# Kernel optimization log

Measured on AMD Instinct MI355X. Metric: run time of the kernel, lower is better.

Reference implementation:

```python
import jax, jax.numpy as jnp
import numpy as np

B, N, DIN, DOUT = 8192, 4, 1024, 256

def setup_inputs() -> dict:
    key = jax.random.key(0)
    k1, k2, k3, k4 = jax.random.split(key, 4)
    adj = jax.random.uniform(k1, (N, N), dtype=jnp.float32)
    features = jax.random.normal(k2, (B, N, DIN), dtype=jnp.float32)
    # nn.Linear(input_size, output_size): weight [DOUT, DIN], bias [DOUT]
    bound = 1.0 / np.sqrt(DIN)
    W = jax.random.uniform(k3, (DOUT, DIN), dtype=jnp.float32, minval=-bound, maxval=bound)
    b = jax.random.uniform(k4, (DOUT,), dtype=jnp.float32, minval=-bound, maxval=bound)
    return {"adj": adj, "features": features, "W": W, "b": b}

def reference(adj, features, W, b):
    # Batched equivalent of: for i in B: linear(adj @ features[i]) -> [B, 4, DOUT]
    h = jnp.einsum("nm,bmf->bnf", adj, features)  # [B, N, DIN]
    return jnp.einsum("bnf,of->bno", h, W) + b    # [B, N, DOUT]
```

## Files before the change

### kernel.cpp

```cpp
#include <hip/hip_runtime.h>


#define DIN 1024
#define DOUT 256
#define BM 32
#define KI 16
#define LDB 72
#define A_HALFS (BM * LDB)

typedef __bf16 bf16x8 __attribute__((ext_vector_type(8)));
typedef float f32x4 __attribute__((ext_vector_type(4)));
typedef unsigned short u16x8 __attribute__((ext_vector_type(8)));

__device__ __forceinline__ unsigned short f2bf(float f) {
  union { float f; unsigned int u; } v;
  v.f = f;
  unsigned int u = v.u;
  u += 0x7fffu + ((u >> 16) & 1u);
  return (unsigned short)(u >> 16);
}

__global__ __launch_bounds__(256) void wprep_kernel(
    const float* __restrict__ W, unsigned short* __restrict__ ws) {
  const int t = blockIdx.x * 256 + threadIdx.x;
  const int lane = t & 63;
  const int j = (t >> 6) & 3;
  const int ks = (t >> 8) & 1;
  const int kb = (t >> 9) & 15;
  const int g = (t >> 13) & 3;
  const int col = g * 64 + j * 16 + (lane & 15);
  const int k0 = kb * 64 + ks * 32 + (lane >> 4) * 8;
  const f32x4* src = (const f32x4*)(W + (size_t)col * DIN + k0);
  f32x4 a = src[0], b = src[1];
  u16x8 pk;
#pragma unroll
  for (int m = 0; m < 4; ++m) {
    pk[m] = f2bf(a[m]);
    pk[4 + m] = f2bf(b[m]);
  }
  *(u16x8*)(ws + (size_t)t * 8) = pk;
}

__global__ __launch_bounds__(256, 4) void gconv_kernel(
    const float* __restrict__ adj, const float* __restrict__ feat,
    const unsigned short* __restrict__ wbf, const float* __restrict__ bias,
    float* __restrict__ out) {
  __shared__ __align__(16) unsigned short sA[2][A_HALFS];

  const int tid = threadIdx.x;
  const int bM = blockIdx.x * BM;

  const int row0 = tid >> 3;
  const int kc8 = (tid & 7) * 8;
  const float* aptr = feat + (size_t)(bM + row0) * DIN + kc8;
  unsigned short* sw0 = &sA[0][row0 * LDB + kc8];
  unsigned short* sw1 = &sA[1][row0 * LDB + kc8];

  const int lane = tid & 63;
  const int wid = tid >> 6;
  const int wc = wid * 64;
  const int rl = lane & 15;
  const int q = lane >> 4;
  const int q8 = q * 8;

  const unsigned short* bp = wbf + (size_t)wid * 128 * 512 + lane * 8;

  f32x4 acc[2][4];
#pragma unroll
  for (int i = 0; i < 2; ++i)
#pragma unroll
    for (int j = 0; j < 4; ++j) acc[i][j] = f32x4{0.f, 0.f, 0.f, 0.f};

  f32x4 pa0 = *(const f32x4*)aptr;
  f32x4 pa1 = *(const f32x4*)(aptr + 4);
  {
    u16x8 pk;
#pragma unroll
    for (int m = 0; m < 4; ++m) {
      pk[m] = f2bf(pa0[m]);
      pk[4 + m] = f2bf(pa1[m]);
    }
    *(u16x8*)sw0 = pk;
  }
  pa0 = *(const f32x4*)(aptr + 64);
  pa1 = *(const f32x4*)(aptr + 68);

  for (int kb = 0; kb < KI; ++kb) {
    bf16x8 bfr[2][4];
#pragma unroll
    for (int ks = 0; ks < 2; ++ks)
#pragma unroll
      for (int j = 0; j < 4; ++j)
        bfr[ks][j] = *(const bf16x8*)(bp + ((kb * 2 + ks) * 4 + j) * 512);

    __builtin_amdgcn_sched_barrier(0);
    asm volatile("s_waitcnt lgkmcnt(0)" ::: "memory");
    __builtin_amdgcn_s_barrier();
    __builtin_amdgcn_sched_barrier(0);

    const unsigned short* sa = (kb & 1) ? &sA[1][0] : &sA[0][0];
#pragma unroll
    for (int ks = 0; ks < 2; ++ks) {
      const int ko = ks * 32 + q8;
      bf16x8 af[2];
#pragma unroll
      for (int i = 0; i < 2; ++i)
        af[i] = *(const bf16x8*)(sa + (i * 16 + rl) * LDB + ko);
#pragma unroll
      for (int i = 0; i < 2; ++i)
#pragma unroll
        for (int j = 0; j < 4; ++j)
          acc[i][j] = __builtin_amdgcn_mfma_f32_16x16x32_bf16(
              af[i], bfr[ks][j], acc[i][j], 0, 0, 0);
    }

    if (kb + 1 < KI) {
      u16x8 pk;
#pragma unroll
      for (int m = 0; m < 4; ++m) {
        pk[m] = f2bf(pa0[m]);
        pk[4 + m] = f2bf(pa1[m]);
      }
      unsigned short* sw = ((kb + 1) & 1) ? sw1 : sw0;
      *(u16x8*)sw = pk;
      if (kb + 2 < KI) {
        const float* a0 = aptr + (size_t)(kb + 2) * 64;
        pa0 = *(const f32x4*)a0;
        pa1 = *(const f32x4*)(a0 + 4);
      }
    }
  }

  float am[16];
#pragma unroll
  for (int i = 0; i < 16; ++i) am[i] = adj[i];

  float bv[4];
#pragma unroll
  for (int j = 0; j < 4; ++j) bv[j] = bias[wc + j * 16 + rl];

#pragma unroll
  for (int i = 0; i < 2; ++i) {
    const size_t rowbase = (size_t)(bM + i * 16 + q * 4);
#pragma unroll
    for (int j = 0; j < 4; ++j) {
      const int col = wc + j * 16 + rl;
      float* op = out + rowbase * DOUT + col;
      f32x4 g = acc[i][j];
#pragma unroll
      for (int n = 0; n < 4; ++n) {
        op[(size_t)n * DOUT] = am[n * 4 + 0] * g[0] + am[n * 4 + 1] * g[1] +
                               am[n * 4 + 2] * g[2] + am[n * 4 + 3] * g[3] +
                               bv[j];
      }
    }
  }
}

extern "C" void kernel_launch(void* const* d_in, const int* in_sizes, int n_in,
                              void* d_out, int out_size, void* d_ws,
                              size_t ws_size, hipStream_t stream) {
  const float* adj = (const float*)d_in[0];
  const float* feat = (const float*)d_in[1];
  const float* W = (const float*)d_in[2];
  const float* bias = (const float*)d_in[3];
  float* out = (float*)d_out;
  unsigned short* ws = (unsigned short*)d_ws;

  wprep_kernel<<<128, 256, 0, stream>>>(W, ws);
  gconv_kernel<<<8192 * 4 / BM, 256, 0, stream>>>(adj, feat, ws, bias, out);
}
```

Baseline: 223.3 us.

## Give each wave a private A tile to remove block-wide barriers

Each wave now loads, converts to bf16, and stores the full 32-row feature tile into its own double-buffered LDS region, so the per-iteration block-wide s_barrier is removed. The intent is to let waves run their MMA loops without synchronizing with each other. In exchange, every block reads and converts the same feature data four times, LDS usage grows fourfold, and launch bounds drop to three blocks per CU.

```diff
diff --git a/kernel.cpp b/kernel.cpp
--- a/kernel.cpp
+++ b/kernel.cpp
@@ -20,6 +20,16 @@
   return (unsigned short)(u >> 16);
 }
 
+__device__ __forceinline__ u16x8 pack8(f32x4 lo, f32x4 hi) {
+  u16x8 r;
+#pragma unroll
+  for (int m = 0; m < 4; ++m) {
+    r[m] = f2bf(lo[m]);
+    r[4 + m] = f2bf(hi[m]);
+  }
+  return r;
+}
+
 __global__ __launch_bounds__(256) void wprep_kernel(
     const float* __restrict__ W, unsigned short* __restrict__ ws) {
   const int t = blockIdx.x * 256 + threadIdx.x;
@@ -32,29 +42,17 @@
   const int k0 = kb * 64 + ks * 32 + (lane >> 4) * 8;
   const f32x4* src = (const f32x4*)(W + (size_t)col * DIN + k0);
   f32x4 a = src[0], b = src[1];
-  u16x8 pk;
-#pragma unroll
-  for (int m = 0; m < 4; ++m) {
-    pk[m] = f2bf(a[m]);
-    pk[4 + m] = f2bf(b[m]);
-  }
-  *(u16x8*)(ws + (size_t)t * 8) = pk;
+  *(u16x8*)(ws + (size_t)t * 8) = pack8(a, b);
 }
 
-__global__ __launch_bounds__(256, 4) void gconv_kernel(
+__global__ __launch_bounds__(256, 3) void gconv_kernel(
     const float* __restrict__ adj, const float* __restrict__ feat,
     const unsigned short* __restrict__ wbf, const float* __restrict__ bias,
     float* __restrict__ out) {
-  __shared__ __align__(16) unsigned short sA[2][A_HALFS];
+  __shared__ __align__(16) unsigned short sA[4][2][A_HALFS];
 
   const int tid = threadIdx.x;
   const int bM = blockIdx.x * BM;
-
-  const int row0 = tid >> 3;
-  const int kc8 = (tid & 7) * 8;
-  const float* aptr = feat + (size_t)(bM + row0) * DIN + kc8;
-  unsigned short* sw0 = &sA[0][row0 * LDB + kc8];
-  unsigned short* sw1 = &sA[1][row0 * LDB + kc8];
 
   const int lane = tid & 63;
   const int wid = tid >> 6;
@@ -62,6 +60,11 @@
   const int rl = lane & 15;
   const int q = lane >> 4;
   const int q8 = q * 8;
+
+  const int arow = lane >> 3;
+  const int ac8 = (lane & 7) * 8;
+  const float* abase = feat + (size_t)(bM + arow) * DIN + ac8;
+  unsigned short* swl = &sA[wid][0][arow * LDB + ac8];
 
   const unsigned short* bp = wbf + (size_t)wid * 128 * 512 + lane * 8;
 
@@ -71,19 +74,20 @@
 #pragma unroll
     for (int j = 0; j < 4; ++j) acc[i][j] = f32x4{0.f, 0.f, 0.f, 0.f};
 
-  f32x4 pa0 = *(const f32x4*)aptr;
-  f32x4 pa1 = *(const f32x4*)(aptr + 4);
-  {
-    u16x8 pk;
+  f32x4 pf[4][2];
 #pragma unroll
-    for (int m = 0; m < 4; ++m) {
-      pk[m] = f2bf(pa0[m]);
-      pk[4 + m] = f2bf(pa1[m]);
-    }
-    *(u16x8*)sw0 = pk;
+  for (int v = 0; v < 4; ++v) {
+    pf[v][0] = *(const f32x4*)(abase + (size_t)v * 8 * DIN);
+    pf[v][1] = *(const f32x4*)(abase + (size_t)v * 8 * DIN + 4);
   }
-  pa0 = *(const f32x4*)(aptr + 64);
-  pa1 = *(const f32x4*)(aptr + 68);
+#pragma unroll
+  for (int v = 0; v < 4; ++v)
+    *(u16x8*)(swl + v * 8 * LDB) = pack8(pf[v][0], pf[v][1]);
+#pragma unroll
+  for (int v = 0; v < 4; ++v) {
+    pf[v][0] = *(const f32x4*)(abase + (size_t)v * 8 * DIN + 64);
+    pf[v][1] = *(const f32x4*)(abase + (size_t)v * 8 * DIN + 68);
+  }
 
   for (int kb = 0; kb < KI; ++kb) {
     bf16x8 bfr[2][4];
@@ -93,40 +97,36 @@
       for (int j = 0; j < 4; ++j)
         bfr[ks][j] = *(const bf16x8*)(bp + ((kb * 2 + ks) * 4 + j) * 512);
 
-    __builtin_amdgcn_sched_barrier(0);
-    asm volatile("s_waitcnt lgkmcnt(0)" ::: "memory");
-    __builtin_amdgcn_s_barrier();
-    __builtin_amdgcn_sched_barrier(0);
+    const unsigned short* sa = &sA[wid][kb & 1][0];
+    bf16x8 af[2][2];
+#pragma unroll
+    for (int i = 0; i < 2; ++i)
+#pragma unroll
+      for (int ks = 0; ks < 2; ++ks)
+        af[i][ks] = *(const bf16x8*)(sa + (i * 16 + rl) * LDB + ks * 32 + q8);
 
-    const unsigned short* sa = (kb & 1) ? &sA[1][0] : &sA[0][0];
 #pragma unroll
-    for (int ks = 0; ks < 2; ++ks) {
-      const int ko = ks * 32 + q8;
-      bf16x8 af[2];
-#pragma unroll
-      for (int i = 0; i < 2; ++i)
-        af[i] = *(const bf16x8*)(sa + (i * 16 + rl) * LDB + ko);
+    for (int ks = 0; ks < 2; ++ks)
 #pragma unroll
       for (int i = 0; i < 2; ++i)
 #pragma unroll
         for (int j = 0; j < 4; ++j)
           acc[i][j] = __builtin_amdgcn_mfma_f32_16x16x32_bf16(
-              af[i], bfr[ks][j], acc[i][j], 0, 0, 0);
-    }
+              af[i][ks], bfr[ks][j], acc[i][j], 0, 0, 0);
 
     if (kb + 1 < KI) {
-      u16x8 pk;
+      unsigned short* sw = swl + ((kb + 1) & 1) * A_HALFS;
 #pragma unroll
-      for (int m = 0; m < 4; ++m) {
-        pk[m] = f2bf(pa0[m]);
-        pk[4 + m] = f2bf(pa1[m]);
-      }
-      unsigned short* sw = ((kb + 1) & 1) ? sw1 : sw0;
-      *(u16x8*)sw = pk;
+      for (int v = 0; v < 4; ++v)
+        *(u16x8*)(sw + v * 8 * LDB) = pack8(pf[v][0], pf[v][1]);
       if (kb + 2 < KI) {
-        const float* a0 = aptr + (size_t)(kb + 2) * 64;
-        pa0 = *(const f32x4*)a0;
-        pa1 = *(const f32x4*)(a0 + 4);
+#pragma unroll
+        for (int v = 0; v < 4; ++v) {
+          pf[v][0] =
+              *(const f32x4*)(abase + (size_t)v * 8 * DIN + (kb + 2) * 64);
+          pf[v][1] =
+              *(const f32x4*)(abase + (size_t)v * 8 * DIN + (kb + 2) * 64 + 4);
+        }
       }
     }
   }
```

Result: slower. 231.4 us (+3.6%).
